# Optimization experiments

Measured on AMD Instinct MI355X. Metric: run time of the kernel, lower is better.

## Reference

```python
import jax, jax.numpy as jnp
import numpy as np

N, D_IN, F = 65536, 512, 256
E = 524288
BATCH, K1 = 32, 200
BN_EPS = 1e-5


def setup_inputs() -> dict:
    key = jax.random.key(0)
    ks = iter(jax.random.split(key, 64))

    def nrm(shape, s=0.05):
        return jax.random.normal(next(ks), shape, jnp.float32) * s

    inp = {
        "feat": jax.random.normal(next(ks), (N, D_IN), jnp.float32),
        "A": jax.random.randint(next(ks), (2, E), 0, N, dtype=jnp.int32),
        "h1id": jax.random.randint(next(ks), (BATCH * K1,), 0, N // BATCH, dtype=jnp.int32),
        "batch": BATCH,
    }
    dims = [(D_IN, F), (F, F), (F, F), (F, F)]
    for i, (di, do) in enumerate(dims, 1):
        inp[f"eps{i}"] = jnp.zeros((), jnp.float32)          # GINConv train_eps, init 0
        inp[f"w{i}a"] = nrm((di, do)); inp[f"b{i}a"] = jnp.zeros((do,), jnp.float32)
        inp[f"w{i}b"] = nrm((do, do)); inp[f"b{i}b"] = jnp.zeros((do,), jnp.float32)
        inp[f"g{i}"] = jnp.ones((do,), jnp.float32)          # BN gamma
        inp[f"be{i}"] = jnp.zeros((do,), jnp.float32)        # BN beta
        inp[f"m{i}"] = nrm((do,))                            # BN running mean
        inp[f"v{i}"] = jax.random.uniform(next(ks), (do,), jnp.float32, 0.5, 1.5)  # BN running var
    inp["wc1"] = nrm((F, F)); inp["bc1"] = jnp.zeros((F,), jnp.float32)
    inp["pa"] = jnp.full((F,), 0.25, jnp.float32)            # PReLU per-channel slope
    inp["wc2"] = nrm((F, 2)); inp["bc2"] = jnp.zeros((2,), jnp.float32)
    return inp


def _gin_conv(x, src, dst, eps, wa, ba, wb, bb, g, be, m, v):
    # sum aggregation over in-edges: aggr[i] = sum_{(j->i)} x[j]
    aggr = jax.ops.segment_sum(x[src], dst, num_segments=N)
    h = (1.0 + eps) * x + aggr
    h = jax.nn.relu(h @ wa + ba) @ wb + bb
    # BatchNorm1d in eval mode (running stats)
    return (h - m) * jax.lax.rsqrt(v + BN_EPS) * g + be


def _forward(feat, A, h1id, batch,
             eps1, w1a, b1a, w1b, b1b, g1, be1, m1, v1,
             eps2, w2a, b2a, w2b, b2b, g2, be2, m2, v2,
             eps3, w3a, b3a, w3b, b3b, g3, be3, m3, v3,
             eps4, w4a, b4a, w4b, b4b, g4, be4, m4, v4,
             wc1, bc1, pa, wc2, bc2):
    src, dst = A[0], A[1]
    h = jax.nn.relu(_gin_conv(feat, src, dst, eps1, w1a, b1a, w1b, b1b, g1, be1, m1, v1))
    h = jax.nn.relu(_gin_conv(h, src, dst, eps2, w2a, b2a, w2b, b2b, g2, be2, m2, v2))
    h = jax.nn.relu(_gin_conv(h, src, dst, eps3, w3a, b3a, w3b, b3b, g3, be3, m3, v3))
    h = _gin_conv(h, src, dst, eps4, w4a, b4a, w4b, b4b, g4, be4, m4, v4)
    score = h.reshape(batch, -1, F)                      # [B, n_per_graph, F]
    idx = h1id.reshape(batch, K1)
    edge_feat = jnp.take_along_axis(score, idx[:, :, None], axis=1)  # [B, K1, F]
    ef = edge_feat.reshape(-1, F)
    hc = ef @ wc1 + bc1
    hc = jnp.where(hc > 0, hc, pa * hc)                  # PReLU(256)
    return hc @ wc2 + bc2                                # [B*K1, 2]


def reference(feat, A, h1id, batch,
              eps1, w1a, b1a, w1b, b1b, g1, be1, m1, v1,
              eps2, w2a, b2a, w2b, b2b, g2, be2, m2, v2,
              eps3, w3a, b3a, w3b, b3b, g3, be3, m3, v3,
              eps4, w4a, b4a, w4b, b4b, g4, be4, m4, v4,
              wc1, bc1, pa, wc2, bc2):
    return _forward(feat, A, h1id, batch,
                    eps1, w1a, b1a, w1b, b1b, g1, be1, m1, v1,
                    eps2, w2a, b2a, w2b, b2b, g2, be2, m2, v2,
                    eps3, w3a, b3a, w3b, b3b, g3, be3, m3, v3,
                    eps4, w4a, b4a, w4b, b4b, g4, be4, m4, v4,
                    wc1, bc1, pa, wc2, bc2)
```

## Files before the change

### kernel.cpp

```cpp
#include <hip/hip_runtime.h>

typedef unsigned short u16;
typedef unsigned int   u32;
typedef __bf16  bf16x8 __attribute__((ext_vector_type(8)));
typedef float   f32x4  __attribute__((ext_vector_type(4)));
typedef u32     u32x4  __attribute__((ext_vector_type(4)));

#define NN 65536
#define NE 524288
#define FD 256

typedef const __attribute__((address_space(1))) void* gas_p;
typedef __attribute__((address_space(3))) void* las_p;
#define GLDS16(g, l) __builtin_amdgcn_global_load_lds((gas_p)(const void*)(g), (las_p)(void*)(l), 16, 0, 0)

__device__ __forceinline__ u16 f2bf(float f){
  u32 u = __float_as_uint(f);
  u += 0x7fffu + ((u >> 16) & 1u);
  return (u16)(u >> 16);
}
__device__ __forceinline__ float bf2f(u32 lo16){
  return __uint_as_float(lo16 << 16);
}
__device__ __forceinline__ void acc8(float* a, uint4 v){
  a[0] += bf2f(v.x & 0xffffu); a[1] += bf2f(v.x >> 16);
  a[2] += bf2f(v.y & 0xffffu); a[3] += bf2f(v.y >> 16);
  a[4] += bf2f(v.z & 0xffffu); a[5] += bf2f(v.z >> 16);
  a[6] += bf2f(v.w & 0xffffu); a[7] += bf2f(v.w >> 16);
}
__device__ __forceinline__ int lsw(int row, int c){
  return row * 256 + ((((c >> 3) ^ (row & 7)) & 31) << 3) + (c & 7);
}

__global__ __launch_bounds__(256) void prep_hist_k(
    const float* __restrict__ w1a, const float* __restrict__ w1b,
    const float* __restrict__ w2a, const float* __restrict__ w2b,
    const float* __restrict__ w3a, const float* __restrict__ w3b,
    const float* __restrict__ w4a, const float* __restrict__ w4b,
    const float* __restrict__ wc1, u16* __restrict__ wT,
    const int* __restrict__ dst, int* __restrict__ deg)
{
  if (blockIdx.x >= 2560){
    int e = (blockIdx.x - 2560) * 256 + threadIdx.x;
    atomicAdd(&deg[dst[e]], 1);
    return;
  }
  int idx = blockIdx.x * 256 + threadIdx.x;
  const float* src; int base, K, local;
  if (idx < 131072){ src = w1a; base = 0; K = 512; local = idx; }
  else {
    local = idx - 131072;
    int j = local >> 16;
    local &= 65535;
    K = 256;
    base = 131072 + j * 65536;
    switch (j){
      case 0: src = w1b; break;
      case 1: src = w2a; break;
      case 2: src = w2b; break;
      case 3: src = w3a; break;
      case 4: src = w3b; break;
      case 5: src = w4a; break;
      case 6: src = w4b; break;
      default: src = wc1; break;
    }
  }
  int n = local & 255;
  int k = local >> 8;
  wT[base + n * K + k] = f2bf(src[k * 256 + n]);
}

__global__ __launch_bounds__(1024) void scan_k(const int* __restrict__ deg, int* __restrict__ rs){
  __shared__ int part[1024];
  int t = threadIdx.x;
  int base = t * 64;
  int sum = 0;
  for (int i = 0; i < 64; ++i) sum += deg[base + i];
  part[t] = sum;
  __syncthreads();
  for (int off = 1; off < 1024; off <<= 1){
    int v = 0;
    if (t >= off) v = part[t - off];
    __syncthreads();
    part[t] += v;
    __syncthreads();
  }
  int run = part[t] - sum;
  for (int i = 0; i < 64; ++i){ rs[base + i] = run; run += deg[base + i]; }
  if (t == 1023) rs[65536] = part[1023];
}

__global__ __launch_bounds__(256) void scat_k(
    const int* __restrict__ src, const int* __restrict__ dst,
    const int* __restrict__ rs, int* __restrict__ cursor, int* __restrict__ csr)
{
  int e = blockIdx.x * 256 + threadIdx.x;
  int d = dst[e];
  int pos = atomicAdd(&cursor[d], 1);
  csr[rs[d] + pos] = src[e];
}

template<int AF32, int MODE, int RELU, int K>
__global__ __launch_bounds__(512) void gemm_k(
    const void* __restrict__ Ap, const u16* __restrict__ Bt,
    u16* __restrict__ C,
    const float* __restrict__ p0, const float* __restrict__ p1,
    const float* __restrict__ p2, const float* __restrict__ p3,
    const float* __restrict__ p4)
{
  __shared__ u16 lds[32768];
  u16* As = lds;
  u16* Bs = lds + 8192;
  const int t    = threadIdx.x;
  const int lane = t & 63;
  const int w    = t >> 6;
  const int wm   = w & 1;
  const int wn   = w >> 1;
  const int m0   = blockIdx.x * 128;
  const int mrow = lane & 15;
  const int quad = lane >> 4;

  f32x4 acc[4][4];
  const f32x4 zero = {0.f, 0.f, 0.f, 0.f};
  #pragma unroll
  for (int i = 0; i < 4; ++i)
    #pragma unroll
    for (int j = 0; j < 4; ++j) acc[i][j] = zero;

  const u16* Ab = (const u16*)Ap;
  const float* Af = (const float*)Ap;

  for (int k0 = 0; k0 < K; k0 += 64){
    if (AF32){
      #pragma unroll
      for (int i = 0; i < 2; ++i){
        int p   = i * 512 + t;
        int row = p >> 3;
        const float* s = Af + (size_t)(m0 + row) * K + k0 + (p & 7) * 8;
        float4 x0 = *(const float4*)s;
        float4 x1 = *(const float4*)(s + 4);
        union { u32x4 q; u16 h[8]; } u;
        u.h[0] = f2bf(x0.x); u.h[1] = f2bf(x0.y); u.h[2] = f2bf(x0.z); u.h[3] = f2bf(x0.w);
        u.h[4] = f2bf(x1.x); u.h[5] = f2bf(x1.y); u.h[6] = f2bf(x1.z); u.h[7] = f2bf(x1.w);
        int dst = (p & ~7) | ((p & 7) ^ (row & 7));
        *(u32x4*)&As[dst * 8] = u.q;
      }
    } else {
      #pragma unroll
      for (int i = 0; i < 2; ++i){
        int p   = i * 512 + t;
        int row = p >> 3;
        int ch  = (p & 7) ^ (row & 7);
        GLDS16(Ab + (size_t)(m0 + row) * K + k0 + ch * 8, &As[p * 8]);
      }
    }
    #pragma unroll
    for (int i = 0; i < 4; ++i){
      int p   = i * 512 + t;
      int row = p >> 3;
      int ch  = (p & 7) ^ (row & 7);
      GLDS16(Bt + (size_t)row * K + k0 + ch * 8, &Bs[p * 8]);
    }
    __syncthreads();
    #pragma unroll
    for (int ks = 0; ks < 2; ++ks){
      bf16x8 af[4], bq[4];
      #pragma unroll
      for (int mi = 0; mi < 4; ++mi){
        int r  = wm * 64 + mi * 16 + mrow;
        int ch = (quad + ks * 4) ^ (r & 7);
        af[mi] = *(const bf16x8*)&As[(r * 8 + ch) * 8];
      }
      #pragma unroll
      for (int ni = 0; ni < 4; ++ni){
        int rb = wn * 64 + ni * 16 + mrow;
        int ch = (quad + ks * 4) ^ (rb & 7);
        bq[ni] = *(const bf16x8*)&Bs[(rb * 8 + ch) * 8];
      }
      #pragma unroll
      for (int mi = 0; mi < 4; ++mi)
        #pragma unroll
        for (int ni = 0; ni < 4; ++ni)
          acc[mi][ni] = __builtin_amdgcn_mfma_f32_16x16x32_bf16(af[mi], bq[ni], acc[mi][ni], 0, 0, 0);
    }
    __syncthreads();
  }

  #pragma unroll
  for (int ni = 0; ni < 4; ++ni){
    int c  = wn * 64 + ni * 16 + mrow;
    float scale = 1.f, shift = 0.f;
    if (MODE == 1){
      float s = p0[c] * rsqrtf(p3[c] + 1e-5f);
      scale = s;
      shift = (p4[c] - p2[c]) * s + p1[c];
    }
    #pragma unroll
    for (int mi = 0; mi < 4; ++mi){
      int rbase = wm * 64 + mi * 16 + quad * 4;
      #pragma unroll
      for (int reg = 0; reg < 4; ++reg){
        float v = acc[mi][ni][reg];
        if (MODE == 1){
          v = v * scale + shift;
          if (RELU) v = fmaxf(v, 0.f);
        }
        lds[lsw(rbase + reg, c)] = f2bf(v);
      }
    }
  }
  __syncthreads();
  #pragma unroll
  for (int i = 0; i < 8; ++i){
    int p  = i * 512 + t;
    int r  = p >> 5;
    int ch = p & 31;
    u32x4 q = *(const u32x4*)&lds[r * 256 + (ch ^ (r & 7)) * 8];
    *(u32x4*)&C[(size_t)(m0 + r) * 256 + ch * 8] = q;
  }
}

__global__ __launch_bounds__(512) void dual_k(
    const u16* __restrict__ Up, const u16* __restrict__ B1t,
    const float* __restrict__ ba,
    const u16* __restrict__ B2t,
    const float* __restrict__ g, const float* __restrict__ be,
    const float* __restrict__ m, const float* __restrict__ v,
    const float* __restrict__ bb,
    u16* __restrict__ C)
{
  __shared__ u16 lds[32768];
  u16* As = lds;
  u16* Bs = lds + 8192;
  const int t    = threadIdx.x;
  const int lane = t & 63;
  const int w    = t >> 6;
  const int wm   = w & 1;
  const int wn   = w >> 1;
  const int m0   = blockIdx.x * 128;
  const int mrow = lane & 15;
  const int quad = lane >> 4;

  const f32x4 zero = {0.f, 0.f, 0.f, 0.f};
  f32x4 acc[4][4];
  #pragma unroll
  for (int i = 0; i < 4; ++i)
    #pragma unroll
    for (int j = 0; j < 4; ++j) acc[i][j] = zero;

  for (int k0 = 0; k0 < 256; k0 += 64){
    #pragma unroll
    for (int i = 0; i < 2; ++i){
      int p   = i * 512 + t;
      int row = p >> 3;
      int ch  = (p & 7) ^ (row & 7);
      GLDS16(Up + (size_t)(m0 + row) * 256 + k0 + ch * 8, &As[p * 8]);
    }
    #pragma unroll
    for (int i = 0; i < 4; ++i){
      int p   = i * 512 + t;
      int row = p >> 3;
      int ch  = (p & 7) ^ (row & 7);
      GLDS16(B1t + (size_t)row * 256 + k0 + ch * 8, &Bs[p * 8]);
    }
    __syncthreads();
    #pragma unroll
    for (int ks = 0; ks < 2; ++ks){
      bf16x8 af[4], bq[4];
      #pragma unroll
      for (int mi = 0; mi < 4; ++mi){
        int r  = wm * 64 + mi * 16 + mrow;
        int ch = (quad + ks * 4) ^ (r & 7);
        af[mi] = *(const bf16x8*)&As[(r * 8 + ch) * 8];
      }
      #pragma unroll
      for (int ni = 0; ni < 4; ++ni){
        int rb = wn * 64 + ni * 16 + mrow;
        int ch = (quad + ks * 4) ^ (rb & 7);
        bq[ni] = *(const bf16x8*)&Bs[(rb * 8 + ch) * 8];
      }
      #pragma unroll
      for (int mi = 0; mi < 4; ++mi)
        #pragma unroll
        for (int ni = 0; ni < 4; ++ni)
          acc[mi][ni] = __builtin_amdgcn_mfma_f32_16x16x32_bf16(af[mi], bq[ni], acc[mi][ni], 0, 0, 0);
    }
    __syncthreads();
  }

  #pragma unroll
  for (int ni = 0; ni < 4; ++ni){
    int c = wn * 64 + ni * 16 + mrow;
    float shift = ba[c];
    #pragma unroll
    for (int mi = 0; mi < 4; ++mi){
      int rbase = wm * 64 + mi * 16 + quad * 4;
      #pragma unroll
      for (int reg = 0; reg < 4; ++reg){
        float val = fmaxf(acc[mi][ni][reg] + shift, 0.f);
        lds[lsw(rbase + reg, c)] = f2bf(val);
      }
    }
  }
  __syncthreads();

  f32x4 acc2[4][4];
  #pragma unroll
  for (int i = 0; i < 4; ++i)
    #pragma unroll
    for (int j = 0; j < 4; ++j) acc2[i][j] = zero;
  #pragma unroll
  for (int ks = 0; ks < 8; ++ks){
    bf16x8 af[4], bq[4];
    #pragma unroll
    for (int mi = 0; mi < 4; ++mi){
      int r    = wm * 64 + mi * 16 + mrow;
      int slot = (ks * 4 + quad) ^ (r & 7);
      af[mi] = *(const bf16x8*)&lds[r * 256 + slot * 8];
    }
    #pragma unroll
    for (int ni = 0; ni < 4; ++ni){
      int rb = wn * 64 + ni * 16 + mrow;
      bq[ni] = *(const bf16x8*)&B2t[(size_t)rb * 256 + ks * 32 + quad * 8];
    }
    #pragma unroll
    for (int mi = 0; mi < 4; ++mi)
      #pragma unroll
      for (int ni = 0; ni < 4; ++ni)
        acc2[mi][ni] = __builtin_amdgcn_mfma_f32_16x16x32_bf16(af[mi], bq[ni], acc2[mi][ni], 0, 0, 0);
  }
  __syncthreads();

  #pragma unroll
  for (int ni = 0; ni < 4; ++ni){
    int c = wn * 64 + ni * 16 + mrow;
    float scale = g[c] * rsqrtf(v[c] + 1e-5f);
    float shift = (bb[c] - m[c]) * scale + be[c];
    #pragma unroll
    for (int mi = 0; mi < 4; ++mi){
      int rbase = wm * 64 + mi * 16 + quad * 4;
      #pragma unroll
      for (int reg = 0; reg < 4; ++reg){
        float val = fmaxf(acc2[mi][ni][reg] * scale + shift, 0.f);
        lds[lsw(rbase + reg, c)] = f2bf(val);
      }
    }
  }
  __syncthreads();
  #pragma unroll
  for (int i = 0; i < 8; ++i){
    int p  = i * 512 + t;
    int r  = p >> 5;
    int ch = p & 31;
    u32x4 q = *(const u32x4*)&lds[r * 256 + (ch ^ (r & 7)) * 8];
    *(u32x4*)&C[(size_t)(m0 + r) * 256 + ch * 8] = q;
  }
}

template<int GATH, int RAW>
__global__ __launch_bounds__(256) void agg_k(
    const u16* __restrict__ y, const int* __restrict__ rs, const int* __restrict__ csr,
    const float* __restrict__ epsp, const float* __restrict__ bias,
    const int* __restrict__ gidx, u16* __restrict__ tout)
{
  int sub    = threadIdx.x >> 5;
  int lane32 = threadIdx.x & 31;
  int idx    = blockIdx.x * 8 + sub;
  int node;
  if (GATH) node = (idx / 200) * 2048 + gidx[idx];
  else      node = idx;
  int f0 = lane32 * 8;
  float e1 = 1.0f + epsp[0];
  int s0 = rs[node], s1 = rs[node + 1];
  uint4 own = *(const uint4*)(y + (size_t)node * 256 + f0);
  float a[8] = {0.f,0.f,0.f,0.f,0.f,0.f,0.f,0.f};
  int e = s0;
  for (; e + 4 <= s1; e += 4){
    int sa = csr[e], sb = csr[e+1], sc = csr[e+2], sd = csr[e+3];
    uint4 va = *(const uint4*)(y + (size_t)sa * 256 + f0);
    uint4 vb = *(const uint4*)(y + (size_t)sb * 256 + f0);
    uint4 vc = *(const uint4*)(y + (size_t)sc * 256 + f0);
    uint4 vd = *(const uint4*)(y + (size_t)sd * 256 + f0);
    acc8(a, va); acc8(a, vb); acc8(a, vc); acc8(a, vd);
  }
  for (; e < s1; ++e){
    int s = csr[e];
    acc8(a, *(const uint4*)(y + (size_t)s * 256 + f0));
  }
  float ow[8];
  ow[0] = bf2f(own.x & 0xffffu); ow[1] = bf2f(own.x >> 16);
  ow[2] = bf2f(own.y & 0xffffu); ow[3] = bf2f(own.y >> 16);
  ow[4] = bf2f(own.z & 0xffffu); ow[5] = bf2f(own.z >> 16);
  ow[6] = bf2f(own.w & 0xffffu); ow[7] = bf2f(own.w >> 16);
  float r[8];
  if (RAW){
    #pragma unroll
    for (int q = 0; q < 8; ++q) r[q] = e1 * ow[q] + a[q];
  } else {
    float4 b0 = *(const float4*)(bias + f0);
    float4 b1 = *(const float4*)(bias + f0 + 4);
    r[0] = fmaxf(e1 * ow[0] + a[0] + b0.x, 0.f);
    r[1] = fmaxf(e1 * ow[1] + a[1] + b0.y, 0.f);
    r[2] = fmaxf(e1 * ow[2] + a[2] + b0.z, 0.f);
    r[3] = fmaxf(e1 * ow[3] + a[3] + b0.w, 0.f);
    r[4] = fmaxf(e1 * ow[4] + a[4] + b1.x, 0.f);
    r[5] = fmaxf(e1 * ow[5] + a[5] + b1.y, 0.f);
    r[6] = fmaxf(e1 * ow[6] + a[6] + b1.z, 0.f);
    r[7] = fmaxf(e1 * ow[7] + a[7] + b1.w, 0.f);
  }
  uint4 o;
  o.x = (u32)f2bf(r[0]) | ((u32)f2bf(r[1]) << 16);
  o.y = (u32)f2bf(r[2]) | ((u32)f2bf(r[3]) << 16);
  o.z = (u32)f2bf(r[4]) | ((u32)f2bf(r[5]) << 16);
  o.w = (u32)f2bf(r[6]) | ((u32)f2bf(r[7]) << 16);
  *(uint4*)(tout + (size_t)idx * 256 + f0) = o;
}

__global__ __launch_bounds__(512) void tail_k(
    const u16* __restrict__ u4p, const u16* __restrict__ w4aT, const float* __restrict__ ba4,
    const u16* __restrict__ w4bT,
    const float* __restrict__ g, const float* __restrict__ be,
    const float* __restrict__ m, const float* __restrict__ v,
    const float* __restrict__ bb,
    const u16* __restrict__ wc1T, const float* __restrict__ bc1, const float* __restrict__ pa,
    const float* __restrict__ wc2, const float* __restrict__ bc2,
    float* __restrict__ out)
{
  __shared__ u16 lds[32768];
  const int t    = threadIdx.x;
  const int lane = t & 63;
  const int w    = t >> 6;
  const int wm   = w & 1;
  const int wn   = w >> 1;
  const int m0   = blockIdx.x * 128;
  const int mrow = lane & 15;
  const int quad = lane >> 4;
  const f32x4 zero = {0.f, 0.f, 0.f, 0.f};

  #pragma unroll
  for (int i = 0; i < 8; ++i){
    int p   = i * 512 + t;
    int row = p >> 5;
    int ch  = (p & 31) ^ (row & 7);
    GLDS16(u4p + (size_t)(m0 + row) * 256 + ch * 8, &lds[p * 8]);
  }
  __syncthreads();

  #pragma unroll 1
  for (int stage = 0; stage < 3; ++stage){
    const u16* Bt = (stage == 0) ? w4aT : (stage == 1) ? w4bT : wc1T;
    f32x4 acc[4][4];
    #pragma unroll
    for (int i = 0; i < 4; ++i)
      #pragma unroll
      for (int j = 0; j < 4; ++j) acc[i][j] = zero;
    #pragma unroll
    for (int ks = 0; ks < 8; ++ks){
      bf16x8 af[4], bq[4];
      #pragma unroll
      for (int mi = 0; mi < 4; ++mi){
        int r    = wm * 64 + mi * 16 + mrow;
        int slot = (ks * 4 + quad) ^ (r & 7);
        af[mi] = *(const bf16x8*)&lds[r * 256 + slot * 8];
      }
      #pragma unroll
      for (int ni = 0; ni < 4; ++ni){
        int rb = wn * 64 + ni * 16 + mrow;
        bq[ni] = *(const bf16x8*)&Bt[(size_t)rb * 256 + ks * 32 + quad * 8];
      }
      #pragma unroll
      for (int mi = 0; mi < 4; ++mi)
        #pragma unroll
        for (int ni = 0; ni < 4; ++ni)
          acc[mi][ni] = __builtin_amdgcn_mfma_f32_16x16x32_bf16(af[mi], bq[ni], acc[mi][ni], 0, 0, 0);
    }
    __syncthreads();
    #pragma unroll
    for (int ni = 0; ni < 4; ++ni){
      int c = wn * 64 + ni * 16 + mrow;
      float scale = 1.f, shift = 0.f, slope = 0.f; int prelu = 0, rel = 0;
      if (stage == 0){ shift = ba4[c]; rel = 1; }
      if (stage == 1){
        float s = g[c] * rsqrtf(v[c] + 1e-5f);
        scale = s;
        shift = (bb[c] - m[c]) * s + be[c];
      }
      if (stage == 2){ shift = bc1[c]; slope = pa[c]; prelu = 1; }
      #pragma unroll
      for (int mi = 0; mi < 4; ++mi){
        int rbase = wm * 64 + mi * 16 + quad * 4;
        #pragma unroll
        for (int reg = 0; reg < 4; ++reg){
          float val = acc[mi][ni][reg] * scale + shift;
          if (rel)   val = fmaxf(val, 0.f);
          if (prelu) val = val > 0.f ? val : slope * val;
          lds[lsw(rbase + reg, c)] = f2bf(val);
        }
      }
    }
    __syncthreads();
  }

  {
    int c0 = lane * 4;
    float4 wva = *(const float4*)(wc2 + c0 * 2);
    float4 wvb = *(const float4*)(wc2 + c0 * 2 + 4);
    float o0 = bc2[0], o1 = bc2[1];
    #pragma unroll 1
    for (int rr = 0; rr < 16; ++rr){
      int row = w * 16 + rr;
      int idxu = row * 256 + (((lane >> 1) ^ (row & 7)) << 3) + (c0 & 7);
      uint2 hv = *(const uint2*)&lds[idxu];
      float h0 = bf2f(hv.x & 0xffffu), h1 = bf2f(hv.x >> 16);
      float h2 = bf2f(hv.y & 0xffffu), h3 = bf2f(hv.y >> 16);
      float a0 = h0 * wva.x + h1 * wva.z + h2 * wvb.x + h3 * wvb.z;
      float a1 = h0 * wva.y + h1 * wva.w + h2 * wvb.y + h3 * wvb.w;
      #pragma unroll
      for (int off = 32; off > 0; off >>= 1){
        a0 += __shfl_xor(a0, off);
        a1 += __shfl_xor(a1, off);
      }
      if (lane == 0){
        out[(m0 + row) * 2]     = a0 + o0;
        out[(m0 + row) * 2 + 1] = a1 + o1;
      }
    }
  }
}

extern "C" void kernel_launch(void* const* d_in, const int* in_sizes, int n_in,
                              void* d_out, int out_size, void* d_ws, size_t ws_size,
                              hipStream_t stream)
{
  const float* feat = (const float*)d_in[0];
  const int*   A    = (const int*)d_in[1];
  const int*   h1id = (const int*)d_in[2];
  const float* eps[4] = {(const float*)d_in[4],  (const float*)d_in[13], (const float*)d_in[22], (const float*)d_in[31]};
  const float* wa [4] = {(const float*)d_in[5],  (const float*)d_in[14], (const float*)d_in[23], (const float*)d_in[32]};
  const float* ba [4] = {(const float*)d_in[6],  (const float*)d_in[15], (const float*)d_in[24], (const float*)d_in[33]};
  const float* wb [4] = {(const float*)d_in[7],  (const float*)d_in[16], (const float*)d_in[25], (const float*)d_in[34]};
  const float* bb [4] = {(const float*)d_in[8],  (const float*)d_in[17], (const float*)d_in[26], (const float*)d_in[35]};
  const float* g  [4] = {(const float*)d_in[9],  (const float*)d_in[18], (const float*)d_in[27], (const float*)d_in[36]};
  const float* be [4] = {(const float*)d_in[10], (const float*)d_in[19], (const float*)d_in[28], (const float*)d_in[37]};
  const float* m  [4] = {(const float*)d_in[11], (const float*)d_in[20], (const float*)d_in[29], (const float*)d_in[38]};
  const float* v  [4] = {(const float*)d_in[12], (const float*)d_in[21], (const float*)d_in[30], (const float*)d_in[39]};
  const float* wc1 = (const float*)d_in[40];
  const float* bc1 = (const float*)d_in[41];
  const float* pa  = (const float*)d_in[42];
  const float* wc2 = (const float*)d_in[43];
  const float* bc2 = (const float*)d_in[44];

  char* ws = (char*)d_ws;
  u16* wT     = (u16*)(ws + 0);
  int* deg    = (int*)(ws + 1310720);
  int* rs     = (int*)(ws + 1572864);
  int* cursor = (int*)(ws + 1835264);
  int* csr    = (int*)(ws + 2097408);
  u16* ybuf   = (u16*)(ws + 4194560);
  u16* tbuf   = (u16*)(ws + 37748992);
  u16* hbuf   = (u16*)(ws + 71303424);
  u16* u4     = (u16*)(ws + 104857856);

  u16* w1aT = wT;
  u16* w1bT = wT + 131072;
  u16* w2aT = wT + 196608;
  u16* w2bT = wT + 262144;
  u16* w3aT = wT + 327680;
  u16* w3bT = wT + 393216;
  u16* w4aT = wT + 458752;
  u16* w4bT = wT + 524288;
  u16* wc1T = wT + 589824;

  hipMemsetAsync(deg, 0, 65536 * 4, stream);
  hipMemsetAsync(cursor, 0, 65536 * 4, stream);
  prep_hist_k<<<4608, 256, 0, stream>>>(wa[0], wb[0], wa[1], wb[1], wa[2], wb[2],
      wa[3], wb[3], wc1, wT, A + NE, deg);
  scan_k<<<1, 1024, 0, stream>>>(deg, rs);
  scat_k<<<NE / 256, 256, 0, stream>>>(A, A + NE, rs, cursor, csr);

  gemm_k<1,0,0,512><<<512, 512, 0, stream>>>(feat, w1aT, ybuf,
      nullptr, nullptr, nullptr, nullptr, nullptr);
  agg_k<0,0><<<NN / 8, 256, 0, stream>>>(ybuf, rs, csr, eps[0], ba[0], nullptr, tbuf);
  gemm_k<0,1,1,256><<<512, 512, 0, stream>>>(tbuf, w1bT, hbuf,
      g[0], be[0], m[0], v[0], bb[0]);

  agg_k<0,1><<<NN / 8, 256, 0, stream>>>(hbuf, rs, csr, eps[1], nullptr, nullptr, ybuf);
  dual_k<<<512, 512, 0, stream>>>(ybuf, w2aT, ba[1], w2bT,
      g[1], be[1], m[1], v[1], bb[1], hbuf);
  agg_k<0,1><<<NN / 8, 256, 0, stream>>>(hbuf, rs, csr, eps[2], nullptr, nullptr, ybuf);
  dual_k<<<512, 512, 0, stream>>>(ybuf, w3aT, ba[2], w3bT,
      g[2], be[2], m[2], v[2], bb[2], hbuf);

  agg_k<1,1><<<800, 256, 0, stream>>>(hbuf, rs, csr, eps[3], nullptr, h1id, u4);
  tail_k<<<50, 512, 0, stream>>>(u4, w4aT, ba[3], w4bT,
      g[3], be[3], m[3], v[3], bb[3],
      wc1T, bc1, pa, wc2, bc2, (float*)d_out);

  (void)in_sizes; (void)n_in; (void)out_size; (void)ws_size;
}
```

Before: 645.2 us.

## Fuse CSR edge scatter into first-layer GEMM launch for concurrent execution

Combines the edge-scatter kernel and the first fp32-input GEMM into one launch. Blocks 0-511 run the GEMM and blocks 512+ do the atomic CSR scatter. The aim is to overlap the latency-bound scatter with the compute-bound GEMM and save one kernel launch. In exchange, the scatter blocks now reserve the same 64KB of LDS as the GEMM blocks, which can limit occupancy. The gemm_k template also loses its fp32-input variant.

```diff
diff --git a/kernel.cpp b/kernel.cpp
--- a/kernel.cpp
+++ b/kernel.cpp
@@ -90,17 +90,107 @@
   if (t == 1023) rs[65536] = part[1023];
 }
 
-__global__ __launch_bounds__(256) void scat_k(
-    const int* __restrict__ src, const int* __restrict__ dst,
+__global__ __launch_bounds__(512) void gemm1_scat_k(
+    const float* __restrict__ Af, const u16* __restrict__ Bt,
+    u16* __restrict__ C,
+    const int* __restrict__ esrc, const int* __restrict__ edst,
     const int* __restrict__ rs, int* __restrict__ cursor, int* __restrict__ csr)
 {
-  int e = blockIdx.x * 256 + threadIdx.x;
-  int d = dst[e];
-  int pos = atomicAdd(&cursor[d], 1);
-  csr[rs[d] + pos] = src[e];
-}
-
-template<int AF32, int MODE, int RELU, int K>
+  __shared__ u16 lds[32768];
+  if (blockIdx.x >= 512){
+    int e = (blockIdx.x - 512) * 512 + threadIdx.x;
+    int d = edst[e];
+    int pos = atomicAdd(&cursor[d], 1);
+    csr[rs[d] + pos] = esrc[e];
+    return;
+  }
+  u16* As = lds;
+  u16* Bs = lds + 8192;
+  const int t    = threadIdx.x;
+  const int lane = t & 63;
+  const int w    = t >> 6;
+  const int wm   = w & 1;
+  const int wn   = w >> 1;
+  const int m0   = blockIdx.x * 128;
+  const int mrow = lane & 15;
+  const int quad = lane >> 4;
+
+  f32x4 acc[4][4];
+  const f32x4 zero = {0.f, 0.f, 0.f, 0.f};
+  #pragma unroll
+  for (int i = 0; i < 4; ++i)
+    #pragma unroll
+    for (int j = 0; j < 4; ++j) acc[i][j] = zero;
+
+  for (int k0 = 0; k0 < 512; k0 += 64){
+    #pragma unroll
+    for (int i = 0; i < 2; ++i){
+      int p   = i * 512 + t;
+      int row = p >> 3;
+      const float* s = Af + (size_t)(m0 + row) * 512 + k0 + (p & 7) * 8;
+      float4 x0 = *(const float4*)s;
+      float4 x1 = *(const float4*)(s + 4);
+      union { u32x4 q; u16 h[8]; } u;
+      u.h[0] = f2bf(x0.x); u.h[1] = f2bf(x0.y); u.h[2] = f2bf(x0.z); u.h[3] = f2bf(x0.w);
+      u.h[4] = f2bf(x1.x); u.h[5] = f2bf(x1.y); u.h[6] = f2bf(x1.z); u.h[7] = f2bf(x1.w);
+      int dst = (p & ~7) | ((p & 7) ^ (row & 7));
+      *(u32x4*)&As[dst * 8] = u.q;
+    }
+    #pragma unroll
+    for (int i = 0; i < 4; ++i){
+      int p   = i * 512 + t;
+      int row = p >> 3;
+      int ch  = (p & 7) ^ (row & 7);
+      GLDS16(Bt + (size_t)row * 512 + k0 + ch * 8, &Bs[p * 8]);
+    }
+    __syncthreads();
+    #pragma unroll
+    for (int ks = 0; ks < 2; ++ks){
+      bf16x8 af[4], bq[4];
+      #pragma unroll
+      for (int mi = 0; mi < 4; ++mi){
+        int r  = wm * 64 + mi * 16 + mrow;
+        int ch = (quad + ks * 4) ^ (r & 7);
+        af[mi] = *(const bf16x8*)&As[(r * 8 + ch) * 8];
+      }
+      #pragma unroll
+      for (int ni = 0; ni < 4; ++ni){
+        int rb = wn * 64 + ni * 16 + mrow;
+        int ch = (quad + ks * 4) ^ (rb & 7);
+        bq[ni] = *(const bf16x8*)&Bs[(rb * 8 + ch) * 8];
+      }
+      #pragma unroll
+      for (int mi = 0; mi < 4; ++mi)
+        #pragma unroll
+        for (int ni = 0; ni < 4; ++ni)
+          acc[mi][ni] = __builtin_amdgcn_mfma_f32_16x16x32_bf16(af[mi], bq[ni], acc[mi][ni], 0, 0, 0);
+    }
+    __syncthreads();
+  }
+
+  #pragma unroll
+  for (int ni = 0; ni < 4; ++ni){
+    int c  = wn * 64 + ni * 16 + mrow;
+    #pragma unroll
+    for (int mi = 0; mi < 4; ++mi){
+      int rbase = wm * 64 + mi * 16 + quad * 4;
+      #pragma unroll
+      for (int reg = 0; reg < 4; ++reg)
+        lds[lsw(rbase + reg, c)] = f2bf(acc[mi][ni][reg]);
+    }
+  }
+  __syncthreads();
+  #pragma unroll
+  for (int i = 0; i < 8; ++i){
+    int p  = i * 512 + t;
+    int r  = p >> 5;
+    int ch = p & 31;
+    u32x4 q = *(const u32x4*)&lds[r * 256 + (ch ^ (r & 7)) * 8];
+    *(u32x4*)&C[(size_t)(m0 + r) * 256 + ch * 8] = q;
+  }
+}
+
+template<int MODE, int RELU, int K>
 __global__ __launch_bounds__(512) void gemm_k(
     const void* __restrict__ Ap, const u16* __restrict__ Bt,
     u16* __restrict__ C,
@@ -128,31 +218,14 @@
     for (int j = 0; j < 4; ++j) acc[i][j] = zero;
 
   const u16* Ab = (const u16*)Ap;
-  const float* Af = (const float*)Ap;
 
   for (int k0 = 0; k0 < K; k0 += 64){
-    if (AF32){
-      #pragma unroll
-      for (int i = 0; i < 2; ++i){
-        int p   = i * 512 + t;
-        int row = p >> 3;
-        const float* s = Af + (size_t)(m0 + row) * K + k0 + (p & 7) * 8;
-        float4 x0 = *(const float4*)s;
-        float4 x1 = *(const float4*)(s + 4);
-        union { u32x4 q; u16 h[8]; } u;
-        u.h[0] = f2bf(x0.x); u.h[1] = f2bf(x0.y); u.h[2] = f2bf(x0.z); u.h[3] = f2bf(x0.w);
-        u.h[4] = f2bf(x1.x); u.h[5] = f2bf(x1.y); u.h[6] = f2bf(x1.z); u.h[7] = f2bf(x1.w);
-        int dst = (p & ~7) | ((p & 7) ^ (row & 7));
-        *(u32x4*)&As[dst * 8] = u.q;
-      }
-    } else {
-      #pragma unroll
-      for (int i = 0; i < 2; ++i){
-        int p   = i * 512 + t;
-        int row = p >> 3;
-        int ch  = (p & 7) ^ (row & 7);
-        GLDS16(Ab + (size_t)(m0 + row) * K + k0 + ch * 8, &As[p * 8]);
-      }
+    #pragma unroll
+    for (int i = 0; i < 2; ++i){
+      int p   = i * 512 + t;
+      int row = p >> 3;
+      int ch  = (p & 7) ^ (row & 7);
+      GLDS16(Ab + (size_t)(m0 + row) * K + k0 + ch * 8, &As[p * 8]);
     }
     #pragma unroll
     for (int i = 0; i < 4; ++i){
@@ -576,12 +649,12 @@
   prep_hist_k<<<4608, 256, 0, stream>>>(wa[0], wb[0], wa[1], wb[1], wa[2], wb[2],
       wa[3], wb[3], wc1, wT, A + NE, deg);
   scan_k<<<1, 1024, 0, stream>>>(deg, rs);
-  scat_k<<<NE / 256, 256, 0, stream>>>(A, A + NE, rs, cursor, csr);
-
-  gemm_k<1,0,0,512><<<512, 512, 0, stream>>>(feat, w1aT, ybuf,
-      nullptr, nullptr, nullptr, nullptr, nullptr);
+
+  gemm1_scat_k<<<1536, 512, 0, stream>>>(feat, w1aT, ybuf,
+      A, A + NE, rs, cursor, csr);
+
   agg_k<0,0><<<NN / 8, 256, 0, stream>>>(ybuf, rs, csr, eps[0], ba[0], nullptr, tbuf);
-  gemm_k<0,1,1,256><<<512, 512, 0, stream>>>(tbuf, w1bT, hbuf,
+  gemm_k<1,1,256><<<512, 512, 0, stream>>>(tbuf, w1bT, hbuf,
       g[0], be[0], m[0], v[0], bb[0]);
 
   agg_k<0,1><<<NN / 8, 256, 0, stream>>>(hbuf, rs, csr, eps[1], nullptr, nullptr, ybuf);
```

After: 636.0 us. About the same (-1.4%).
